# Kernel tuning notes

Hardware: AMD Instinct MI355X
Metric: run time of the kernel (lower is better)

The kernel has to match this reference:

```python
import jax, jax.numpy as jnp
import numpy as np

# Irreps layout: x = [32x0e | 16x1o] -> dim 32 + 48 = 80; sh = [1x0e | 1x1o] -> dim 4
MUL0, MUL1 = 32, 16
DIM = MUL0 + 3 * MUL1            # 80
E, N = 100000, 10000             # edges, nodes
EDGE_DIM, HIDDEN = 32, 64
# e3nn instruction order (i_in1 outer, i_in2 inner):
#   A: 0e x 0e -> 0e  (MUL0*MUL0)
#   C: 0e x 1o -> 1o  (MUL0*MUL1)
#   D: 1o x 0e -> 1o  (MUL1*MUL1)
#   B: 1o x 1o -> 0e  (MUL1*MUL0)
NA = MUL0 * MUL0
NC = MUL0 * MUL1
ND = MUL1 * MUL1
NB = MUL1 * MUL0
WNUM = NA + NC + ND + NB         # tp.weight_numel = 2304
INV_SQRT3 = 1.0 / np.sqrt(3.0).astype(np.float32)   # CG (1,1,0) = delta/sqrt(3)
NORM = np.float32(1.0 / np.sqrt(MUL0 + MUL1))        # element path norm: fan-in = 32+16 = 48 for both outputs


def setup_inputs() -> dict:
    key = jax.random.key(0)
    ks = jax.random.split(key, 10)
    return {
        "dst": jax.random.randint(ks[0], (E,), 0, N),
        "x_src": jax.random.normal(ks[1], (E, DIM), jnp.float32),
        "x_dst": jax.random.normal(ks[2], (N, DIM), jnp.float32),
        "sh": jax.random.normal(ks[3], (E, 4), jnp.float32),
        "edge_attr": jax.random.normal(ks[4], (E, EDGE_DIM), jnp.float32),
        "mlp_w1": jax.random.normal(ks[5], (EDGE_DIM, HIDDEN), jnp.float32) / np.sqrt(EDGE_DIM),
        "mlp_b1": jnp.zeros((HIDDEN,), jnp.float32),
        "mlp_w2": jax.random.normal(ks[6], (HIDDEN, WNUM), jnp.float32) / np.sqrt(HIDDEN),
        "mlp_b2": jnp.zeros((WNUM,), jnp.float32),
        "res_w0": jax.random.normal(ks[7], (MUL0, MUL0), jnp.float32),
        "res_w1": jax.random.normal(ks[8], (MUL1, MUL1), jnp.float32),
    }


def reference(dst, x_src, x_dst, sh, edge_attr, mlp_w1, mlp_b1, mlp_w2, mlp_b2, res_w0, res_w1):
    e = x_src.shape[0]
    n = x_dst.shape[0]
    # edge MLP -> per-edge tensor-product weights
    h = jax.nn.relu(edge_attr @ mlp_w1 + mlp_b1)
    w = h @ mlp_w2 + mlp_b2                              # [E, WNUM]
    wa = w[:, :NA].reshape(e, MUL0, MUL0)                # 0e x 0e -> 0e
    wc = w[:, NA:NA + NC].reshape(e, MUL0, MUL1)         # 0e x 1o -> 1o
    wd = w[:, NA + NC:NA + NC + ND].reshape(e, MUL1, MUL1)  # 1o x 0e -> 1o
    wb = w[:, NA + NC + ND:].reshape(e, MUL1, MUL0)      # 1o x 1o -> 0e

    x0 = x_src[:, :MUL0]                                 # [E, 32]
    x1 = x_src[:, MUL0:].reshape(e, MUL1, 3)             # [E, 16, 3]
    sh0 = sh[:, 0]                                       # [E]
    sh1 = sh[:, 1:4]                                     # [E, 3]

    # equivariant tensor product with per-edge weights
    out0 = NORM * (jnp.einsum('euw,eu,e->ew', wa, x0, sh0)
                   + INV_SQRT3 * jnp.einsum('euw,eum,em->ew', wb, x1, sh1))   # [E, 32]
    out1 = NORM * (jnp.einsum('euw,eu,em->ewm', wc, x0, sh1)
                   + jnp.einsum('euw,eum,e->ewm', wd, x1, sh0))               # [E, 16, 3]
    msg = jnp.concatenate([out0, out1.reshape(e, 3 * MUL1)], axis=-1)        # [E, 80]

    # scatter-mean to destination nodes
    sums = jax.ops.segment_sum(msg, dst, num_segments=n)                      # [N, 80]
    cnt = jax.ops.segment_sum(jnp.ones((e,), msg.dtype), dst, num_segments=n)
    mean = sums / jnp.maximum(cnt, 1.0)[:, None]

    # residual: e3nn Linear (per-irrep, fan-in normalized)
    r0 = (x_dst[:, :MUL0] @ res_w0) / np.sqrt(MUL0)
    r1 = jnp.einsum('num,uw->nwm', x_dst[:, MUL0:].reshape(n, MUL1, 3), res_w1) / np.sqrt(MUL1)
    res = jnp.concatenate([r0, r1.reshape(n, 3 * MUL1)], axis=-1)

    return res + mean
```

## Files before the change

### kernel.cpp

```cpp
#include <hip/hip_runtime.h>
#include <hip/hip_bf16.h>

#define E_TOT   100000
#define N_NODES 10000
#define DIMV    80
#define HID     64
#define EDIM    32
#define WNUM    2304
#define TE      32

static constexpr float NORMF      = 0.14433756729740643f;
static constexpr float INV_SQRT3F = 0.57735026918962576f;
static constexpr float RS32       = 0.17677669529663687f;
static constexpr float RS16       = 0.25f;

typedef __attribute__((ext_vector_type(8))) short bf16x8;
typedef __attribute__((ext_vector_type(4))) float f32x4;

static __device__ __forceinline__ ushort f2bf(float v) {
    __hip_bfloat16 h(v);
    return *reinterpret_cast<ushort*>(&h);
}

__global__ __launch_bounds__(256) void prep_w2t(const float* __restrict__ W2,
                                                ushort* __restrict__ W2T) {
    int idx = blockIdx.x * 256 + threadIdx.x;
    if (idx >= WNUM * HID) return;
    int j = idx >> 6, t = idx & 63;
    W2T[idx] = f2bf(W2[t * WNUM + j]);
}

__global__ __launch_bounds__(256) void edge_kernel(
    const int* __restrict__ dst, const float* __restrict__ x_src,
    const float* __restrict__ sh, const float* __restrict__ ea,
    const float* __restrict__ W1, const float* __restrict__ b1,
    const ushort* __restrict__ W2T, const float* __restrict__ b2,
    float* __restrict__ sums, float* __restrict__ cnt)
{
    __shared__ float  sX[TE][DIMV];
    __shared__ float  sSh[TE][4];
    __shared__ float  sXs1[TE][16];
    __shared__ float  cA[TE][32];
    __shared__ ushort sHbf[TE][HID];
    __shared__ float  sB2[WNUM];
    __shared__ float  sMsg[TE][84];
    __shared__ int    sDst[TE];
    __shared__ float  sEa[TE][EDIM];

    const int tid  = threadIdx.x;
    const int lane = tid & 63;
    const int wave = tid >> 6;
    const int e0   = blockIdx.x * TE;

    for (int i = tid; i < TE*DIMV; i += 256) sX[0][i]  = x_src[e0*DIMV + i];
    for (int i = tid; i < TE*EDIM; i += 256) sEa[0][i] = ea[e0*EDIM + i];
    for (int i = tid; i < TE*4;    i += 256) sSh[0][i] = sh[e0*4 + i];
    for (int i = tid; i < WNUM;    i += 256) sB2[i]    = b2[i];
    if (tid < TE) sDst[tid] = dst[e0 + tid];
    __syncthreads();

    #pragma unroll
    for (int k = 0; k < (TE*HID)/256; ++k) {
        int idx = tid + k*256;
        int e = idx >> 6, t = idx & 63;
        float h = b1[t];
        #pragma unroll
        for (int i = 0; i < EDIM; ++i) h = fmaf(sEa[e][i], W1[i*HID + t], h);
        sHbf[e][t] = f2bf(fmaxf(h, 0.f));
    }
    for (int i = tid; i < TE*32; i += 256) {
        int e = i >> 5, u = i & 31;
        cA[e][u] = sSh[e][0] * sX[e][u];
    }
    for (int i = tid; i < TE*16; i += 256) {
        int e = i >> 4, u = i & 15;
        sXs1[e][u] = INV_SQRT3F * (sX[e][32+u*3+0]*sSh[e][1] +
                                   sX[e][32+u*3+1]*sSh[e][2] +
                                   sX[e][32+u*3+2]*sSh[e][3]);
    }
    for (int i = tid; i < TE*84; i += 256) sMsg[0][i] = 0.f;
    __syncthreads();

    const int c     = lane & 15;
    const int g     = lane >> 4;
    const int rbase = g << 2;
    bf16x8 afrag[2][2];
    #pragma unroll
    for (int rt = 0; rt < 2; ++rt)
        #pragma unroll
        for (int kt = 0; kt < 2; ++kt)
            afrag[rt][kt] = *reinterpret_cast<const bf16x8*>(&sHbf[rt*16 + c][kt*32 + g*8]);

    float pA[8]    = {};
    float sC2[8]   = {};
    float sDv[8][3] = {};

    for (int t16 = wave; t16 < 144; t16 += 4) {
        const int j0 = t16 << 4;
        const ushort* bp = W2T + ((size_t)(j0 + c) << 6) + g*8;
        bf16x8 bf0 = *reinterpret_cast<const bf16x8*>(bp);
        bf16x8 bf1 = *reinterpret_cast<const bf16x8*>(bp + 32);
        f32x4 acc0 = {0.f, 0.f, 0.f, 0.f};
        f32x4 acc1 = {0.f, 0.f, 0.f, 0.f};
        acc0 = __builtin_amdgcn_mfma_f32_16x16x32_bf16(afrag[0][0], bf0, acc0, 0, 0, 0);
        acc0 = __builtin_amdgcn_mfma_f32_16x16x32_bf16(afrag[0][1], bf1, acc0, 0, 0, 0);
        acc1 = __builtin_amdgcn_mfma_f32_16x16x32_bf16(afrag[1][0], bf0, acc1, 0, 0, 0);
        acc1 = __builtin_amdgcn_mfma_f32_16x16x32_bf16(afrag[1][1], bf1, acc1, 0, 0, 0);
        const float bv = sB2[j0 + c];

        if (t16 < 64) {
            const int u = t16 >> 1;
            #pragma unroll
            for (int r = 0; r < 4; ++r) {
                pA[r]   = fmaf(cA[rbase + r][u],      acc0[r] + bv, pA[r]);
                pA[4+r] = fmaf(cA[16 + rbase + r][u], acc1[r] + bv, pA[4+r]);
            }
        } else if (t16 < 96) {
            const int u = t16 - 64;
            #pragma unroll
            for (int r = 0; r < 4; ++r) {
                sC2[r]   = fmaf(sX[rbase + r][u],      acc0[r] + bv, sC2[r]);
                sC2[4+r] = fmaf(sX[16 + rbase + r][u], acc1[r] + bv, sC2[4+r]);
            }
        } else if (t16 < 112) {
            const int u = t16 - 96;
            #pragma unroll
            for (int r = 0; r < 4; ++r) {
                const float v0 = acc0[r] + bv;
                const float v1 = acc1[r] + bv;
                #pragma unroll
                for (int m = 0; m < 3; ++m) {
                    sDv[r][m]   = fmaf(sX[rbase + r][32 + u*3 + m],      v0, sDv[r][m]);
                    sDv[4+r][m] = fmaf(sX[16 + rbase + r][32 + u*3 + m], v1, sDv[4+r][m]);
                }
            }
        } else {
            const int u = (t16 - 112) >> 1;
            #pragma unroll
            for (int r = 0; r < 4; ++r) {
                pA[r]   = fmaf(sXs1[rbase + r][u],      acc0[r] + bv, pA[r]);
                pA[4+r] = fmaf(sXs1[16 + rbase + r][u], acc1[r] + bv, pA[4+r]);
            }
        }
    }

    const int wcol = c + ((wave & 1) << 4);
    #pragma unroll
    for (int rt = 0; rt < 2; ++rt) {
        #pragma unroll
        for (int r = 0; r < 4; ++r) {
            const int e = rt*16 + rbase + r;
            const int s = rt*4 + r;
            atomicAdd(&sMsg[e][wcol], pA[s]);
            const float s0 = sSh[e][0];
            atomicAdd(&sMsg[e][32 + c*3 + 0], sSh[e][1]*sC2[s] + s0*sDv[s][0]);
            atomicAdd(&sMsg[e][32 + c*3 + 1], sSh[e][2]*sC2[s] + s0*sDv[s][1]);
            atomicAdd(&sMsg[e][32 + c*3 + 2], sSh[e][3]*sC2[s] + s0*sDv[s][2]);
        }
    }
    __syncthreads();

    for (int i = tid; i < TE*DIMV; i += 256) {
        int e = i / DIMV, k = i - e*DIMV;
        atomicAdd(&sums[sDst[e]*DIMV + k], NORMF * sMsg[e][k]);
    }
    if (tid < TE) atomicAdd(&cnt[sDst[tid]], 1.0f);
}

__global__ __launch_bounds__(256) void node_kernel(
    const float* __restrict__ x_dst, const float* __restrict__ rw0,
    const float* __restrict__ rw1, const float* __restrict__ sums,
    const float* __restrict__ cnt, float* __restrict__ out)
{
    int gid = blockIdx.x*256 + threadIdx.x;
    if (gid >= N_NODES*DIMV) return;
    int n = gid / DIMV;
    int k = gid - n*DIMV;
    const float* xd = x_dst + n*DIMV;
    float r = 0.f;
    if (k < 32) {
        #pragma unroll
        for (int u = 0; u < 32; ++u) r = fmaf(xd[u], rw0[u*32 + k], r);
        r *= RS32;
    } else {
        int kk = k - 32;
        int w = kk / 3, m = kk - w*3;
        #pragma unroll
        for (int u = 0; u < 16; ++u) r = fmaf(xd[32 + u*3 + m], rw1[u*16 + w], r);
        r *= RS16;
    }
    float cc = cnt[n];
    out[gid] = r + sums[gid] / fmaxf(cc, 1.f);
}

extern "C" void kernel_launch(void* const* d_in, const int* in_sizes, int n_in,
                              void* d_out, int out_size, void* d_ws, size_t ws_size,
                              hipStream_t stream) {
    const int*   dst   = (const int*)  d_in[0];
    const float* x_src = (const float*)d_in[1];
    const float* x_dst = (const float*)d_in[2];
    const float* sh    = (const float*)d_in[3];
    const float* ea    = (const float*)d_in[4];
    const float* W1    = (const float*)d_in[5];
    const float* b1    = (const float*)d_in[6];
    const float* W2    = (const float*)d_in[7];
    const float* b2    = (const float*)d_in[8];
    const float* rw0   = (const float*)d_in[9];
    const float* rw1   = (const float*)d_in[10];
    float* out  = (float*)d_out;

    float*  sums = (float*)d_ws;
    float*  cnt  = sums + (size_t)N_NODES*DIMV;
    ushort* W2T  = (ushort*)((char*)d_ws + (size_t)(N_NODES*DIMV + N_NODES)*sizeof(float));

    hipMemsetAsync(d_ws, 0, (size_t)(N_NODES*DIMV + N_NODES)*sizeof(float), stream);
    prep_w2t<<<(WNUM*HID + 255)/256, 256, 0, stream>>>(W2, W2T);
    edge_kernel<<<E_TOT/TE, 256, 0, stream>>>(dst, x_src, sh, ea, W1, b1, W2T, b2, sums, cnt);
    node_kernel<<<(N_NODES*DIMV + 255)/256, 256, 0, stream>>>(x_dst, rw0, rw1, sums, cnt, out);
}
```

Measured before the change: 454.4 us.

## Cut edge-kernel LDS, split tile loop by path, transpose W2 via shared memory

Removes the shared b2 copy and reuses one LDS buffer for both edge attributes and the sh0-scaled x0, which shrinks the edge kernel's shared-memory footprint. It also pads the LDS arrays against bank conflicts and adds a launch-bounds occupancy hint. The branchy tile loop becomes four straight loops, one per tensor-product path, and the bias is folded into the MFMA accumulator init. The W2 transpose now goes through a shared-memory tile so both reads and writes are coalesced. The cost is an extra barrier, and the occupancy hint may force register spills.

```diff
diff --git a/kernel.cpp b/kernel.cpp
--- a/kernel.cpp
+++ b/kernel.cpp
@@ -24,38 +24,46 @@
 
 __global__ __launch_bounds__(256) void prep_w2t(const float* __restrict__ W2,
                                                 ushort* __restrict__ W2T) {
-    int idx = blockIdx.x * 256 + threadIdx.x;
-    if (idx >= WNUM * HID) return;
-    int j = idx >> 6, t = idx & 63;
-    W2T[idx] = f2bf(W2[t * WNUM + j]);
-}
-
-__global__ __launch_bounds__(256) void edge_kernel(
+    __shared__ float sT[64][65];
+    const int j0 = blockIdx.x * 64;
+    #pragma unroll
+    for (int k = 0; k < 16; ++k) {
+        int idx = threadIdx.x + k*256;
+        int t = idx >> 6, j = idx & 63;
+        sT[j][t] = W2[t*WNUM + j0 + j];
+    }
+    __syncthreads();
+    #pragma unroll
+    for (int k = 0; k < 16; ++k) {
+        int idx = threadIdx.x + k*256;
+        int j = idx >> 6, t = idx & 63;
+        W2T[(size_t)(j0 + j)*64 + t] = f2bf(sT[j][t]);
+    }
+}
+
+__global__ __launch_bounds__(256, 4) void edge_kernel(
     const int* __restrict__ dst, const float* __restrict__ x_src,
     const float* __restrict__ sh, const float* __restrict__ ea,
     const float* __restrict__ W1, const float* __restrict__ b1,
     const ushort* __restrict__ W2T, const float* __restrict__ b2,
     float* __restrict__ sums, float* __restrict__ cnt)
 {
-    __shared__ float  sX[TE][DIMV];
+    __shared__ float  sX[TE][81];
     __shared__ float  sSh[TE][4];
-    __shared__ float  sXs1[TE][16];
-    __shared__ float  cA[TE][32];
+    __shared__ float  sXs1[TE][17];
+    __shared__ float  sEcA[TE][33];
     __shared__ ushort sHbf[TE][HID];
-    __shared__ float  sB2[WNUM];
     __shared__ float  sMsg[TE][84];
     __shared__ int    sDst[TE];
-    __shared__ float  sEa[TE][EDIM];
 
     const int tid  = threadIdx.x;
     const int lane = tid & 63;
     const int wave = tid >> 6;
     const int e0   = blockIdx.x * TE;
 
-    for (int i = tid; i < TE*DIMV; i += 256) sX[0][i]  = x_src[e0*DIMV + i];
-    for (int i = tid; i < TE*EDIM; i += 256) sEa[0][i] = ea[e0*EDIM + i];
+    for (int i = tid; i < TE*DIMV; i += 256) { int e = i/80, k = i-e*80; sX[e][k] = x_src[e0*DIMV + i]; }
+    for (int i = tid; i < TE*EDIM; i += 256) { int e = i>>5, k = i&31; sEcA[e][k] = ea[e0*EDIM + i]; }
     for (int i = tid; i < TE*4;    i += 256) sSh[0][i] = sh[e0*4 + i];
-    for (int i = tid; i < WNUM;    i += 256) sB2[i]    = b2[i];
     if (tid < TE) sDst[tid] = dst[e0 + tid];
     __syncthreads();
 
@@ -65,12 +73,14 @@
         int e = idx >> 6, t = idx & 63;
         float h = b1[t];
         #pragma unroll
-        for (int i = 0; i < EDIM; ++i) h = fmaf(sEa[e][i], W1[i*HID + t], h);
+        for (int i = 0; i < EDIM; ++i) h = fmaf(sEcA[e][i], W1[i*HID + t], h);
         sHbf[e][t] = f2bf(fmaxf(h, 0.f));
     }
+    __syncthreads();
+
     for (int i = tid; i < TE*32; i += 256) {
         int e = i >> 5, u = i & 31;
-        cA[e][u] = sSh[e][0] * sX[e][u];
+        sEcA[e][u] = sSh[e][0] * sX[e][u];
     }
     for (int i = tid; i < TE*16; i += 256) {
         int e = i >> 4, u = i & 15;
@@ -91,56 +101,69 @@
         for (int kt = 0; kt < 2; ++kt)
             afrag[rt][kt] = *reinterpret_cast<const bf16x8*>(&sHbf[rt*16 + c][kt*32 + g*8]);
 
-    float pA[8]    = {};
-    float sC2[8]   = {};
+    float pA[8]     = {};
+    float sC2[8]    = {};
     float sDv[8][3] = {};
 
-    for (int t16 = wave; t16 < 144; t16 += 4) {
+    auto tile_mfma = [&](int t16, f32x4& a0, f32x4& a1) {
         const int j0 = t16 << 4;
-        const ushort* bp = W2T + ((size_t)(j0 + c) << 6) + g*8;
+        const ushort* bp = W2T + (((size_t)(j0 + c)) << 6) + (g << 3);
         bf16x8 bf0 = *reinterpret_cast<const bf16x8*>(bp);
         bf16x8 bf1 = *reinterpret_cast<const bf16x8*>(bp + 32);
-        f32x4 acc0 = {0.f, 0.f, 0.f, 0.f};
-        f32x4 acc1 = {0.f, 0.f, 0.f, 0.f};
-        acc0 = __builtin_amdgcn_mfma_f32_16x16x32_bf16(afrag[0][0], bf0, acc0, 0, 0, 0);
-        acc0 = __builtin_amdgcn_mfma_f32_16x16x32_bf16(afrag[0][1], bf1, acc0, 0, 0, 0);
-        acc1 = __builtin_amdgcn_mfma_f32_16x16x32_bf16(afrag[1][0], bf0, acc1, 0, 0, 0);
-        acc1 = __builtin_amdgcn_mfma_f32_16x16x32_bf16(afrag[1][1], bf1, acc1, 0, 0, 0);
-        const float bv = sB2[j0 + c];
-
-        if (t16 < 64) {
-            const int u = t16 >> 1;
+        const float bv = b2[j0 + c];
+        a0 = {bv, bv, bv, bv};
+        a1 = {bv, bv, bv, bv};
+        a0 = __builtin_amdgcn_mfma_f32_16x16x32_bf16(afrag[0][0], bf0, a0, 0, 0, 0);
+        a0 = __builtin_amdgcn_mfma_f32_16x16x32_bf16(afrag[0][1], bf1, a0, 0, 0, 0);
+        a1 = __builtin_amdgcn_mfma_f32_16x16x32_bf16(afrag[1][0], bf0, a1, 0, 0, 0);
+        a1 = __builtin_amdgcn_mfma_f32_16x16x32_bf16(afrag[1][1], bf1, a1, 0, 0, 0);
+    };
+
+    #pragma unroll 2
+    for (int k = 0; k < 16; ++k) {
+        const int t16 = wave + (k << 2);
+        f32x4 a0, a1; tile_mfma(t16, a0, a1);
+        const int u = t16 >> 1;
+        #pragma unroll
+        for (int r = 0; r < 4; ++r) {
+            pA[r]   = fmaf(sEcA[rbase + r][u],      a0[r], pA[r]);
+            pA[4+r] = fmaf(sEcA[16 + rbase + r][u], a1[r], pA[4+r]);
+        }
+    }
+    #pragma unroll 2
+    for (int k = 0; k < 8; ++k) {
+        const int t16 = 64 + wave + (k << 2);
+        f32x4 a0, a1; tile_mfma(t16, a0, a1);
+        const int u = t16 - 64;
+        #pragma unroll
+        for (int r = 0; r < 4; ++r) {
+            sC2[r]   = fmaf(sX[rbase + r][u],      a0[r], sC2[r]);
+            sC2[4+r] = fmaf(sX[16 + rbase + r][u], a1[r], sC2[4+r]);
+        }
+    }
+    #pragma unroll
+    for (int k = 0; k < 4; ++k) {
+        const int t16 = 96 + wave + (k << 2);
+        f32x4 a0, a1; tile_mfma(t16, a0, a1);
+        const int u = t16 - 96;
+        #pragma unroll
+        for (int r = 0; r < 4; ++r) {
             #pragma unroll
-            for (int r = 0; r < 4; ++r) {
-                pA[r]   = fmaf(cA[rbase + r][u],      acc0[r] + bv, pA[r]);
-                pA[4+r] = fmaf(cA[16 + rbase + r][u], acc1[r] + bv, pA[4+r]);
+            for (int m = 0; m < 3; ++m) {
+                sDv[r][m]   = fmaf(sX[rbase + r][32 + u*3 + m],      a0[r], sDv[r][m]);
+                sDv[4+r][m] = fmaf(sX[16 + rbase + r][32 + u*3 + m], a1[r], sDv[4+r][m]);
             }
-        } else if (t16 < 96) {
-            const int u = t16 - 64;
-            #pragma unroll
-            for (int r = 0; r < 4; ++r) {
-                sC2[r]   = fmaf(sX[rbase + r][u],      acc0[r] + bv, sC2[r]);
-                sC2[4+r] = fmaf(sX[16 + rbase + r][u], acc1[r] + bv, sC2[4+r]);
-            }
-        } else if (t16 < 112) {
-            const int u = t16 - 96;
-            #pragma unroll
-            for (int r = 0; r < 4; ++r) {
-                const float v0 = acc0[r] + bv;
-                const float v1 = acc1[r] + bv;
-                #pragma unroll
-                for (int m = 0; m < 3; ++m) {
-                    sDv[r][m]   = fmaf(sX[rbase + r][32 + u*3 + m],      v0, sDv[r][m]);
-                    sDv[4+r][m] = fmaf(sX[16 + rbase + r][32 + u*3 + m], v1, sDv[4+r][m]);
-                }
-            }
-        } else {
-            const int u = (t16 - 112) >> 1;
-            #pragma unroll
-            for (int r = 0; r < 4; ++r) {
-                pA[r]   = fmaf(sXs1[rbase + r][u],      acc0[r] + bv, pA[r]);
-                pA[4+r] = fmaf(sXs1[16 + rbase + r][u], acc1[r] + bv, pA[4+r]);
-            }
+        }
+    }
+    #pragma unroll 2
+    for (int k = 0; k < 8; ++k) {
+        const int t16 = 112 + wave + (k << 2);
+        f32x4 a0, a1; tile_mfma(t16, a0, a1);
+        const int u = (t16 - 112) >> 1;
+        #pragma unroll
+        for (int r = 0; r < 4; ++r) {
+            pA[r]   = fmaf(sXs1[rbase + r][u],      a0[r], pA[r]);
+            pA[4+r] = fmaf(sXs1[16 + rbase + r][u], a1[r], pA[4+r]);
         }
     }
 
@@ -214,7 +237,7 @@
     ushort* W2T  = (ushort*)((char*)d_ws + (size_t)(N_NODES*DIMV + N_NODES)*sizeof(float));
 
     hipMemsetAsync(d_ws, 0, (size_t)(N_NODES*DIMV + N_NODES)*sizeof(float), stream);
-    prep_w2t<<<(WNUM*HID + 255)/256, 256, 0, stream>>>(W2, W2T);
+    prep_w2t<<<WNUM/64, 256, 0, stream>>>(W2, W2T);
     edge_kernel<<<E_TOT/TE, 256, 0, stream>>>(dst, x_src, sh, ea, W1, b1, W2T, b2, sums, cnt);
     node_kernel<<<(N_NODES*DIMV + 255)/256, 256, 0, stream>>>(x_dst, rw0, rw1, sums, cnt, out);
 }
```

After: 423.5 us. -6.8%, faster.
